# Kernel optimization log

Measured on AMD Instinct MI355X. Metric: run time of the kernel, lower is better.

Reference implementation:

```python
import jax, jax.numpy as jnp
import numpy as np

INPUT_SIZE = 256
HIDDEN_SIZE = 512


def setup_inputs() -> dict:
    key = jax.random.key(0)
    ks = jax.random.split(key, 8)
    N, L = 128, 1024
    bound_cell = 1.0 / np.sqrt(HIDDEN_SIZE)
    bound_fc = 1.0 / np.sqrt(HIDDEN_SIZE)
    u = lambda k, shape, b: jax.random.uniform(k, shape, jnp.float32, -b, b)
    return {
        "x": jax.random.normal(ks[0], (N, L, INPUT_SIZE), jnp.float32),
        "h": jnp.zeros((N, HIDDEN_SIZE), jnp.float32),
        "W_ih": u(ks[1], (HIDDEN_SIZE, INPUT_SIZE), bound_cell),
        "W_hh": u(ks[2], (HIDDEN_SIZE, HIDDEN_SIZE), bound_cell),
        "b_ih": u(ks[3], (HIDDEN_SIZE,), bound_cell),
        "b_hh": u(ks[4], (HIDDEN_SIZE,), bound_cell),
        "W_out": u(ks[5], (HIDDEN_SIZE, HIDDEN_SIZE), bound_fc),
        "b_out": u(ks[6], (HIDDEN_SIZE,), bound_fc),
    }


def reference(x, h, W_ih, W_hh, b_ih, b_hh, W_out, b_out):
    # Precompute input projections for all timesteps in one big GEMM: [N,L,H]
    xp = jnp.einsum("nli,hi->nlh", x, W_ih) + b_ih + b_hh

    def step(h, xp_t):
        h = jnp.tanh(xp_t + h @ W_hh.T)
        return h, None

    # scan over time: xp transposed to [L,N,H]
    h, _ = jax.lax.scan(step, h, jnp.swapaxes(xp, 0, 1))
    y = h @ W_out.T + b_out
    return (y, h)
```

## Files before the change

### kernel.cpp

```cpp
#include <hip/hip_runtime.h>

typedef _Float16 f16;
typedef _Float16 f16x2 __attribute__((ext_vector_type(2)));
typedef _Float16 f16x4 __attribute__((ext_vector_type(4)));
typedef _Float16 f16x8 __attribute__((ext_vector_type(8)));
typedef float    f32x4 __attribute__((ext_vector_type(4)));

static __device__ __forceinline__ float dot4(uint4 w, uint4 h, float acc) {
    acc = __builtin_amdgcn_fdot2(__builtin_bit_cast(f16x2, w.x), __builtin_bit_cast(f16x2, h.x), acc, false);
    acc = __builtin_amdgcn_fdot2(__builtin_bit_cast(f16x2, w.y), __builtin_bit_cast(f16x2, h.y), acc, false);
    acc = __builtin_amdgcn_fdot2(__builtin_bit_cast(f16x2, w.z), __builtin_bit_cast(f16x2, h.z), acc, false);
    acc = __builtin_amdgcn_fdot2(__builtin_bit_cast(f16x2, w.w), __builtin_bit_cast(f16x2, h.w), acc, false);
    return acc;
}

static __device__ __forceinline__ float dppx1(float v) {
    int r = __builtin_amdgcn_mov_dpp(__builtin_bit_cast(int, v), 0xB1, 0xF, 0xF, true);
    return __builtin_bit_cast(float, r);
}
static __device__ __forceinline__ float dppx2(float v) {
    int r = __builtin_amdgcn_mov_dpp(__builtin_bit_cast(int, v), 0x4E, 0xF, 0xF, true);
    return __builtin_bit_cast(float, r);
}

static __device__ __forceinline__ int hswz(int j) {
    int ig = j >> 6;
    return ig * 64 + ((((j >> 3) & 7) ^ ig) << 3) + (j & 7);
}

__global__ __launch_bounds__(256) void cvt_w(const float4* __restrict__ wih4,
                                             const float4* __restrict__ whh4,
                                             f16x4* __restrict__ wih16,
                                             f16x4* __restrict__ whh16) {
    int idx = blockIdx.x * 256 + threadIdx.x;
    if (idx < 32768) {
        float4 v = wih4[idx];
        wih16[idx] = (f16x4){(f16)v.x, (f16)v.y, (f16)v.z, (f16)v.w};
    } else if (idx < 98304) {
        int k = idx - 32768;
        float4 v = whh4[k];
        whh16[k] = (f16x4){(f16)v.x, (f16)v.y, (f16)v.z, (f16)v.w};
    }
}

__global__ __launch_bounds__(256) void gemm_xp(const float* __restrict__ x,
                                               const f16* __restrict__ wih,
                                               const float* __restrict__ bih,
                                               const float* __restrict__ bhh,
                                               f16* __restrict__ xp,
                                               int tc, int t0, int L) {
    __shared__ f16 As[128][48];
    __shared__ f16 Bs[128][48];
    int tid = threadIdx.x;
    int r = tid >> 1, kh = (tid & 1) * 16;

    long mbase = (long)blockIdx.x * 128;
    int jb = blockIdx.y * 128;
    long mp = mbase + r;
    int n = (int)(mp / tc);
    int trel = (int)(mp - (long)n * tc);
    const float* xrow = x + ((long)n * L + t0 + trel) * 256 + kh;
    const f16* wrow = wih + (jb + r) * 256 + kh;

    int w = tid >> 6, l = tid & 63, lr = l & 15, lk = l >> 4;
    int wm = w & 1, wn = w >> 1;

    f32x4 acc[4][4] = {};

    for (int kk = 0; kk < 256; kk += 32) {
        float4 a0 = *(const float4*)(xrow + kk);
        float4 a1 = *(const float4*)(xrow + kk + 4);
        float4 a2 = *(const float4*)(xrow + kk + 8);
        float4 a3 = *(const float4*)(xrow + kk + 12);
        uint4  b0 = *(const uint4*)(wrow + kk);
        uint4  b1 = *(const uint4*)(wrow + kk + 8);
        f16x8 ca = {(f16)a0.x,(f16)a0.y,(f16)a0.z,(f16)a0.w,(f16)a1.x,(f16)a1.y,(f16)a1.z,(f16)a1.w};
        f16x8 cb = {(f16)a2.x,(f16)a2.y,(f16)a2.z,(f16)a2.w,(f16)a3.x,(f16)a3.y,(f16)a3.z,(f16)a3.w};
        __syncthreads();
        *(f16x8*)&As[r][kh]     = ca;
        *(f16x8*)&As[r][kh + 8] = cb;
        *(uint4*)&Bs[r][kh]     = b0;
        *(uint4*)&Bs[r][kh + 8] = b1;
        __syncthreads();

        uint4 af[4], bf[4];
#pragma unroll
        for (int mi = 0; mi < 4; ++mi) af[mi] = *(const uint4*)&As[wm * 64 + mi * 16 + lr][lk * 8];
#pragma unroll
        for (int ni = 0; ni < 4; ++ni) bf[ni] = *(const uint4*)&Bs[wn * 64 + ni * 16 + lr][lk * 8];
#pragma unroll
        for (int mi = 0; mi < 4; ++mi)
#pragma unroll
            for (int ni = 0; ni < 4; ++ni)
                acc[mi][ni] = __builtin_amdgcn_mfma_f32_16x16x32_f16(
                    __builtin_bit_cast(f16x8, af[mi]), __builtin_bit_cast(f16x8, bf[ni]),
                    acc[mi][ni], 0, 0, 0);
    }

#pragma unroll
    for (int ni = 0; ni < 4; ++ni) {
        int j = jb + wn * 64 + ni * 16 + lr;
        float bias = bih[j] + bhh[j];
#pragma unroll
        for (int mi = 0; mi < 4; ++mi) {
            long row = mbase + wm * 64 + mi * 16 + lk * 4;
#pragma unroll
            for (int rr = 0; rr < 4; ++rr)
                xp[(row + rr) * 512 + j] = (f16)(acc[mi][ni][rr] + bias);
        }
    }
}

__global__ __attribute__((amdgpu_flat_work_group_size(512, 512),
                          amdgpu_waves_per_eu(2, 2)))
void rnn_seq(const f16* __restrict__ whh16,
             const f16* __restrict__ xp,
             const float* __restrict__ hin,
             float* __restrict__ out,
             const float* __restrict__ wout,
             const float* __restrict__ bout,
             int tc, int finalflag, int ytotal) {
    __shared__ uint4 WL[8192];
    __shared__ f16 hb[2][512];
    __shared__ f16 xb[2][512];

    int tid = threadIdx.x;
    int n = blockIdx.x;
    int i = tid & 7;
    int jg = tid >> 3;
    int sx = (i >> 2) & 1;
    int wlbase = (jg * 64 + i) * 2;

    uint4 wr[8][6];
    const f16* wbase = whh16 + (long)(jg * 8) * 512 + i * 64;
#pragma unroll
    for (int jj = 0; jj < 8; ++jj) {
        const uint4* p = (const uint4*)(wbase + jj * 512);
#pragma unroll
        for (int v = 0; v < 6; ++v) wr[jj][v] = p[v];
        uint4 c0 = p[6], c1 = p[7];
        WL[wlbase + jj * 16 + sx]       = c0;
        WL[wlbase + jj * 16 + (1 - sx)] = c1;
    }

    hb[0][hswz(tid)] = (f16)hin[n * 512 + tid];
    const f16* xprow = xp + (long)n * tc * 512;
    if (tid < 64) *(uint4*)&xb[0][tid * 8] = *(const uint4*)(xprow + tid * 8);
    __syncthreads();

    int jfin = jg * 8 + (((i & 1) << 2) | (i & 2) | ((i >> 2) & 1));
    int hw = hswz(jfin);
    float lasth = 0.f;
    int cur = 0;

    for (int t = 0; t < tc; ++t) {
        uint4 pf;
        int dop = (tid < 64) && (t + 1 < tc);
        if (dop) pf = *(const uint4*)(xprow + (long)(t + 1) * 512 + tid * 8);

        const uint4* hcb = ((const uint4*)&hb[cur][0]) + i * 8;
        float a[8];
#pragma unroll
        for (int jj = 0; jj < 8; ++jj) a[jj] = 0.f;

        uint4 h0 = hcb[0 ^ i], h1 = hcb[1 ^ i], h2 = hcb[2 ^ i];
#pragma unroll
        for (int jj = 0; jj < 8; ++jj) {
            a[jj] = dot4(wr[jj][0], h0, a[jj]);
            a[jj] = dot4(wr[jj][1], h1, a[jj]);
            a[jj] = dot4(wr[jj][2], h2, a[jj]);
        }
        h0 = hcb[3 ^ i]; h1 = hcb[4 ^ i]; h2 = hcb[5 ^ i];
#pragma unroll
        for (int jj = 0; jj < 8; ++jj) {
            a[jj] = dot4(wr[jj][3], h0, a[jj]);
            a[jj] = dot4(wr[jj][4], h1, a[jj]);
            a[jj] = dot4(wr[jj][5], h2, a[jj]);
        }
        h0 = hcb[6 ^ i]; h1 = hcb[7 ^ i];
#pragma unroll
        for (int jj = 0; jj < 8; ++jj) {
            uint4 wa = WL[wlbase + jj * 16 + sx];
            uint4 wb = WL[wlbase + jj * 16 + (1 - sx)];
            a[jj] = dot4(wa, h0, a[jj]);
            a[jj] = dot4(wb, h1, a[jj]);
        }

#pragma unroll
        for (int s = 0; s < 4; ++s) {
            float lo = a[s], hi = a[s + 4];
            float keep = (i & 1) ? hi : lo, send = (i & 1) ? lo : hi;
            a[s] = keep + dppx1(send);
        }
#pragma unroll
        for (int s = 0; s < 2; ++s) {
            float lo = a[s], hi = a[s + 2];
            float keep = (i & 2) ? hi : lo, send = (i & 2) ? lo : hi;
            a[s] = keep + dppx2(send);
        }
        {
            float lo = a[0], hi = a[1];
            float keep = (i & 4) ? hi : lo, send = (i & 4) ? lo : hi;
            a[0] = keep + __shfl_xor(send, 4);
        }

        float xv = (float)xb[cur][jfin];
        float pre = a[0] + xv;
        pre = fminf(fmaxf(pre, -20.f), 20.f);
        float e = __expf(2.f * pre);
        float hn = 1.f - 2.f / (e + 1.f);
        lasth = hn;
        hb[cur ^ 1][hw] = (f16)hn;
        if (dop) *(uint4*)&xb[cur ^ 1][tid * 8] = pf;
        __syncthreads();
        cur ^= 1;
    }

    out[ytotal + n * 512 + jfin] = lasth;

    if (finalflag) {
        float* hf = (float*)&xb[0][0];
        hf[jfin] = lasth;
        __syncthreads();
        int jy = tid;
        float acc = bout[jy];
        const float* wrp = wout + (long)jy * 512;
#pragma unroll 4
        for (int k = 0; k < 512; k += 8) {
            float4 w0 = *(const float4*)(wrp + k);
            float4 w1 = *(const float4*)(wrp + k + 4);
            float4 g0 = *(const float4*)(hf + k);
            float4 g1 = *(const float4*)(hf + k + 4);
            acc = fmaf(w0.x, g0.x, acc); acc = fmaf(w0.y, g0.y, acc);
            acc = fmaf(w0.z, g0.z, acc); acc = fmaf(w0.w, g0.w, acc);
            acc = fmaf(w1.x, g1.x, acc); acc = fmaf(w1.y, g1.y, acc);
            acc = fmaf(w1.z, g1.z, acc); acc = fmaf(w1.w, g1.w, acc);
        }
        out[n * 512 + jy] = acc;
    }
}

extern "C" void kernel_launch(void* const* d_in, const int* in_sizes, int n_in,
                              void* d_out, int out_size, void* d_ws, size_t ws_size,
                              hipStream_t stream) {
    const float* x    = (const float*)d_in[0];
    const float* h0   = (const float*)d_in[1];
    const float* wih  = (const float*)d_in[2];
    const float* whh  = (const float*)d_in[3];
    const float* bih  = (const float*)d_in[4];
    const float* bhh  = (const float*)d_in[5];
    const float* wout = (const float*)d_in[6];
    const float* bout = (const float*)d_in[7];
    float* out = (float*)d_out;

    int N = in_sizes[1] / 512;
    int L = (int)((long)in_sizes[0] / ((long)N * 256));
    int ytotal = N * 512;

    char* ws = (char*)d_ws;
    f16* whh16 = (f16*)ws;
    f16* wih16 = (f16*)(ws + 524288);
    f16* xp    = (f16*)(ws + 786432);
    long per_t = (long)N * 512 * 2;
    long cap = (ws_size > 786432) ? (long)(ws_size - 786432) : 0;
    long Tc = cap / per_t;
    if (Tc > L) Tc = L;
    if (Tc < 1) Tc = 1;

    cvt_w<<<384, 256, 0, stream>>>((const float4*)wih, (const float4*)whh,
                                   (f16x4*)wih16, (f16x4*)whh16);

    for (int t0 = 0; t0 < L;) {
        int tc = (int)((L - t0 < Tc) ? (L - t0) : Tc);
        gemm_xp<<<dim3(tc, 4), 256, 0, stream>>>(x, wih16, bih, bhh, xp, tc, t0, L);
        const float* hsrc = (t0 == 0) ? h0 : (const float*)(out + ytotal);
        int fin = (t0 + tc == L) ? 1 : 0;
        rnn_seq<<<N, 512, 0, stream>>>(whh16, xp, hsrc, out, wout, bout, tc, fin, ytotal);
        t0 += tc;
    }
}
```

Before: 1.624 ms.

## Split recurrent matvec across 1024 threads per sequence with padded h buffer

Doubles the threads per block in the recurrent kernel so each thread handles a 32-wide k-slice instead of 64. This halves per-thread register weights and dot work per timestep, at the cost of an extra cross-lane reduction step. The h buffer now uses a padded layout to avoid bank conflicts, replacing the XOR swizzle. The x-projection prefetch through shared memory is replaced by a direct per-thread global load each step. Larger blocks mean more waves to synchronise at the per-step barrier, and the direct loads put global memory latency on the critical path.

Result: slower. 1.997 ms (+23.0%).

```diff
diff --git a/kernel.cpp b/kernel.cpp
--- a/kernel.cpp
+++ b/kernel.cpp
@@ -21,11 +21,6 @@
 static __device__ __forceinline__ float dppx2(float v) {
     int r = __builtin_amdgcn_mov_dpp(__builtin_bit_cast(int, v), 0x4E, 0xF, 0xF, true);
     return __builtin_bit_cast(float, r);
-}
-
-static __device__ __forceinline__ int hswz(int j) {
-    int ig = j >> 6;
-    return ig * 64 + ((((j >> 3) & 7) ^ ig) << 3) + (j & 7);
 }
 
 __global__ __launch_bounds__(256) void cvt_w(const float4* __restrict__ wih4,
@@ -111,79 +106,61 @@
     }
 }
 
-__global__ __attribute__((amdgpu_flat_work_group_size(512, 512),
-                          amdgpu_waves_per_eu(2, 2)))
-void rnn_seq(const f16* __restrict__ whh16,
-             const f16* __restrict__ xp,
-             const float* __restrict__ hin,
-             float* __restrict__ out,
-             const float* __restrict__ wout,
-             const float* __restrict__ bout,
-             int tc, int finalflag, int ytotal) {
+__global__ __launch_bounds__(1024) void rnn_seq(const f16* __restrict__ whh16,
+                                                const f16* __restrict__ xp,
+                                                const float* __restrict__ hin,
+                                                float* __restrict__ out,
+                                                const float* __restrict__ wout,
+                                                const float* __restrict__ bout,
+                                                int tc, int finalflag, int ytotal) {
     __shared__ uint4 WL[8192];
-    __shared__ f16 hb[2][512];
-    __shared__ f16 xb[2][512];
-
-    int tid = threadIdx.x;
-    int n = blockIdx.x;
-    int i = tid & 7;
-    int jg = tid >> 3;
-    int sx = (i >> 2) & 1;
-    int wlbase = (jg * 64 + i) * 2;
-
-    uint4 wr[8][6];
-    const f16* wbase = whh16 + (long)(jg * 8) * 512 + i * 64;
-#pragma unroll
-    for (int jj = 0; jj < 8; ++jj) {
-        const uint4* p = (const uint4*)(wbase + jj * 512);
-#pragma unroll
-        for (int v = 0; v < 6; ++v) wr[jj][v] = p[v];
-        uint4 c0 = p[6], c1 = p[7];
-        WL[wlbase + jj * 16 + sx]       = c0;
-        WL[wlbase + jj * 16 + (1 - sx)] = c1;
-    }
-
-    hb[0][hswz(tid)] = (f16)hin[n * 512 + tid];
-    const f16* xprow = xp + (long)n * tc * 512;
-    if (tid < 64) *(uint4*)&xb[0][tid * 8] = *(const uint4*)(xprow + tid * 8);
+    __shared__ uint4 hbuf[2][80];
+
+    const int tid = threadIdx.x;
+    const int n = blockIdx.x;
+    const int i  = tid & 15;
+    const int jg = tid >> 4;
+    const int sw = tid & 7;
+
+    uint4 wr[8][3];
+    const f16* wbase = whh16 + (long)(jg * 8) * 512 + i * 32;
+#pragma unroll
+    for (int r = 0; r < 8; ++r) {
+        const uint4* p = (const uint4*)(wbase + (long)r * 512);
+        wr[r][0] = p[0]; wr[r][1] = p[1]; wr[r][2] = p[2];
+        WL[tid * 8 + (r ^ sw)] = p[3];
+    }
+
+    if (tid < 512) {
+        int j = tid;
+        ((f16*)&hbuf[0][0])[((j >> 5) * 5 + ((j >> 3) & 3)) * 8 + (j & 7)] =
+            (f16)hin[n * 512 + j];
+    }
     __syncthreads();
 
-    int jfin = jg * 8 + (((i & 1) << 2) | (i & 2) | ((i >> 2) & 1));
-    int hw = hswz(jfin);
+    const int jrow = ((i & 1) << 2) | (i & 2) | ((i >> 2) & 1);
+    const int jfin = jg * 8 + jrow;
+    const int widx = ((jfin >> 5) * 5 + ((jfin >> 3) & 3)) * 8 + (jfin & 7);
+    const f16* xpp = xp + ((long)n * tc) * 512 + jfin;
+    const int wbyte = tid * 128 + sw * 16;
+
     float lasth = 0.f;
     int cur = 0;
 
     for (int t = 0; t < tc; ++t) {
-        uint4 pf;
-        int dop = (tid < 64) && (t + 1 < tc);
-        if (dop) pf = *(const uint4*)(xprow + (long)(t + 1) * 512 + tid * 8);
-
-        const uint4* hcb = ((const uint4*)&hb[cur][0]) + i * 8;
+        float xv = (float)xpp[(long)t * 512];
+
+        const uint4* hrow = &hbuf[cur][i * 5];
+        uint4 hv0 = hrow[0], hv1 = hrow[1], hv2 = hrow[2], hv3 = hrow[3];
+
         float a[8];
 #pragma unroll
-        for (int jj = 0; jj < 8; ++jj) a[jj] = 0.f;
-
-        uint4 h0 = hcb[0 ^ i], h1 = hcb[1 ^ i], h2 = hcb[2 ^ i];
-#pragma unroll
-        for (int jj = 0; jj < 8; ++jj) {
-            a[jj] = dot4(wr[jj][0], h0, a[jj]);
-            a[jj] = dot4(wr[jj][1], h1, a[jj]);
-            a[jj] = dot4(wr[jj][2], h2, a[jj]);
-        }
-        h0 = hcb[3 ^ i]; h1 = hcb[4 ^ i]; h2 = hcb[5 ^ i];
-#pragma unroll
-        for (int jj = 0; jj < 8; ++jj) {
-            a[jj] = dot4(wr[jj][3], h0, a[jj]);
-            a[jj] = dot4(wr[jj][4], h1, a[jj]);
-            a[jj] = dot4(wr[jj][5], h2, a[jj]);
-        }
-        h0 = hcb[6 ^ i]; h1 = hcb[7 ^ i];
-#pragma unroll
-        for (int jj = 0; jj < 8; ++jj) {
-            uint4 wa = WL[wlbase + jj * 16 + sx];
-            uint4 wb = WL[wlbase + jj * 16 + (1 - sx)];
-            a[jj] = dot4(wa, h0, a[jj]);
-            a[jj] = dot4(wb, h1, a[jj]);
+        for (int r = 0; r < 8; ++r)
+            a[r] = dot4(wr[r][2], hv2, dot4(wr[r][1], hv1, dot4(wr[r][0], hv0, 0.f)));
+#pragma unroll
+        for (int r = 0; r < 8; ++r) {
+            uint4 wl = *(const uint4*)((const char*)WL + (wbyte ^ (r << 4)));
+            a[r] = dot4(wl, hv3, a[r]);
         }
 
 #pragma unroll
@@ -203,15 +180,14 @@
             float keep = (i & 4) ? hi : lo, send = (i & 4) ? lo : hi;
             a[0] = keep + __shfl_xor(send, 4);
         }
-
-        float xv = (float)xb[cur][jfin];
+        a[0] += __shfl_xor(a[0], 8);
+
         float pre = a[0] + xv;
         pre = fminf(fmaxf(pre, -20.f), 20.f);
         float e = __expf(2.f * pre);
         float hn = 1.f - 2.f / (e + 1.f);
         lasth = hn;
-        hb[cur ^ 1][hw] = (f16)hn;
-        if (dop) *(uint4*)&xb[cur ^ 1][tid * 8] = pf;
+        ((f16*)&hbuf[cur ^ 1][0])[widx] = (f16)hn;
         __syncthreads();
         cur ^= 1;
     }
@@ -219,24 +195,27 @@
     out[ytotal + n * 512 + jfin] = lasth;
 
     if (finalflag) {
-        float* hf = (float*)&xb[0][0];
+        __syncthreads();
+        float* hf = (float*)WL;
         hf[jfin] = lasth;
         __syncthreads();
-        int jy = tid;
-        float acc = bout[jy];
-        const float* wrp = wout + (long)jy * 512;
+        if (tid < 512) {
+            int jy = tid;
+            float acc = bout[jy];
+            const float* wrp = wout + (long)jy * 512;
 #pragma unroll 4
-        for (int k = 0; k < 512; k += 8) {
-            float4 w0 = *(const float4*)(wrp + k);
-            float4 w1 = *(const float4*)(wrp + k + 4);
-            float4 g0 = *(const float4*)(hf + k);
-            float4 g1 = *(const float4*)(hf + k + 4);
-            acc = fmaf(w0.x, g0.x, acc); acc = fmaf(w0.y, g0.y, acc);
-            acc = fmaf(w0.z, g0.z, acc); acc = fmaf(w0.w, g0.w, acc);
-            acc = fmaf(w1.x, g1.x, acc); acc = fmaf(w1.y, g1.y, acc);
-            acc = fmaf(w1.z, g1.z, acc); acc = fmaf(w1.w, g1.w, acc);
-        }
-        out[n * 512 + jy] = acc;
+            for (int k = 0; k < 512; k += 8) {
+                float4 w0 = *(const float4*)(wrp + k);
+                float4 w1 = *(const float4*)(wrp + k + 4);
+                float4 g0 = *(const float4*)(hf + k);
+                float4 g1 = *(const float4*)(hf + k + 4);
+                acc = fmaf(w0.x, g0.x, acc); acc = fmaf(w0.y, g0.y, acc);
+                acc = fmaf(w0.z, g0.z, acc); acc = fmaf(w0.w, g0.w, acc);
+                acc = fmaf(w1.x, g1.x, acc); acc = fmaf(w1.y, g1.y, acc);
+                acc = fmaf(w1.z, g1.z, acc); acc = fmaf(w1.w, g1.w, acc);
+            }
+            out[n * 512 + jy] = acc;
+        }
     }
 }
 
@@ -275,7 +254,7 @@
         gemm_xp<<<dim3(tc, 4), 256, 0, stream>>>(x, wih16, bih, bhh, xp, tc, t0, L);
         const float* hsrc = (t0 == 0) ? h0 : (const float*)(out + ytotal);
         int fin = (t0 + tc == L) ? 1 : 0;
-        rnn_seq<<<N, 512, 0, stream>>>(whh16, xp, hsrc, out, wout, bout, tc, fin, ytotal);
+        rnn_seq<<<N, 1024, 0, stream>>>(whh16, xp, hsrc, out, wout, bout, tc, fin, ytotal);
         t0 += tc;
     }
 }
```
